# Kernel tuning notes

Measured on AMD Instinct MI355X. Metric: run time of the kernel, lower is better.

Reference implementation:

```python
import jax, jax.numpy as jnp
import numpy as np

N = 100000      # nodes
E = 1600000     # directed edges (before self loops)
F_IN = 128      # n_features
H = 100         # hidden width of every GCNConv / fc1
N_HIDDEN = 8    # conv2..conv9


def setup_inputs() -> dict:
    key = jax.random.key(0)
    ks = jax.random.split(key, 12)
    s = 0.05
    x = jax.random.normal(ks[0], (N, F_IN), jnp.float32)
    edge_index = jax.random.randint(ks[1], (2, E), 0, N, dtype=jnp.int64)
    labels = (jax.random.uniform(ks[2], (N, 1)) < 0.1).astype(jnp.float32)
    W1 = jax.random.normal(ks[3], (F_IN, H), jnp.float32) * s
    b1 = jnp.zeros((H,), jnp.float32)
    Wh = jax.random.normal(ks[4], (N_HIDDEN, H, H), jnp.float32) * s
    bh = jnp.zeros((N_HIDDEN, H), jnp.float32)
    fc1_W = jax.random.normal(ks[5], (H, H), jnp.float32) * s
    fc1_b = jnp.zeros((H,), jnp.float32)
    fc2_W = jax.random.normal(ks[6], (H, 1), jnp.float32) * s
    fc2_b = jnp.zeros((1,), jnp.float32)
    return {"x": x, "edge_index": edge_index, "labels": labels,
            "W1": W1, "b1": b1, "Wh": Wh, "bh": bh,
            "fc1_W": fc1_W, "fc1_b": fc1_b, "fc2_W": fc2_W, "fc2_b": fc2_b}


def _gcn_conv(h, W, b, src, dst, norm):
    # linear transform, then degree-normalized scatter aggregation (PyG GCNConv)
    h = h @ W                                   # [N, H]
    msg = h[src] * norm[:, None]                # [E2, H] gather + scale
    agg = jax.ops.segment_sum(msg, dst, num_segments=N)  # scatter-add to [N, H]
    return agg + b


def reference(x, edge_index, labels, W1, b1, Wh, bh, fc1_W, fc1_b, fc2_W, fc2_b):
    # GCN normalization with self loops: norm_e = deg^-1/2[src] * deg^-1/2[dst]
    loops = jnp.arange(N, dtype=edge_index.dtype)
    src = jnp.concatenate([edge_index[0], loops])
    dst = jnp.concatenate([edge_index[1], loops])
    deg = jax.ops.segment_sum(jnp.ones_like(dst, jnp.float32), dst, num_segments=N)
    dinv = jax.lax.rsqrt(deg)                   # deg >= 1 due to self loops
    norm = dinv[src] * dinv[dst]

    # NOTE: source uses x.relu() (out-of-place, discarded) -> no nonlinearity;
    # dropout is identity in eval mode. Faithful reproduction below.
    h = _gcn_conv(x, W1, b1, src, dst, norm)
    for i in range(N_HIDDEN):
        h = _gcn_conv(h, Wh[i], bh[i], src, dst, norm)

    h = h @ fc1_W + fc1_b
    logits = h @ fc2_W + fc2_b
    p = jax.nn.sigmoid(logits)                  # [N, 1]

    # generate_weights: upweight positives by neg/pos ratio
    pos = labels.sum()
    w = ((jnp.float32(N) - pos) / pos) * labels + 1.0

    pc = jnp.clip(p, 1e-7, 1.0 - 1e-7)
    bce = -(labels * jnp.log(pc) + (1.0 - labels) * jnp.log(1.0 - pc))
    loss = jnp.mean(w * bce)
    return loss, p
```

## Files before the change

### kernel.cpp

```cpp
#include <hip/hip_runtime.h>
#include <hip/hip_fp16.h>
#include <math.h>

#define HW 100
#define FIN 128
#define NBLK 256
#define TPB 1024
#define CHUNK 392
#define PBLK 500
#define SLICE 3200
#define SL4 800
#define ELDS 7424
#define M17 0x1FFFFu
#define NPADH 100352
#define HSPLIT 50048
#define HV40 6256
#define HV41 6244

typedef int iv4 __attribute__((ext_vector_type(4)));

__device__ __forceinline__ float ld_dev(const float* p) {
    return __hip_atomic_load(p, __ATOMIC_RELAXED, __HIP_MEMORY_SCOPE_AGENT);
}
__device__ __forceinline__ unsigned ld_devu(const unsigned* p) {
    return __hip_atomic_load(p, __ATOMIC_RELAXED, __HIP_MEMORY_SCOPE_AGENT);
}
__device__ __forceinline__ void st_devu(unsigned* p, unsigned v) {
    __hip_atomic_store(p, v, __ATOMIC_RELAXED, __HIP_MEMORY_SCOPE_AGENT);
}
__device__ __forceinline__ void st_devh(__half* p, __half v) {
    __hip_atomic_store(reinterpret_cast<unsigned short*>(p),
                       *reinterpret_cast<unsigned short*>(&v),
                       __ATOMIC_RELAXED, __HIP_MEMORY_SCOPE_AGENT);
}

__global__ __launch_bounds__(256) void k_prep(const int* __restrict__ src,
                                              const int* __restrict__ dst,
                                              unsigned* __restrict__ buckets,
                                              int* __restrict__ cntG, int* __restrict__ ofsG,
                                              float* __restrict__ accums,
                                              unsigned* __restrict__ posDone,
                                              unsigned* __restrict__ fin,
                                              unsigned* __restrict__ flags,
                                              const float* __restrict__ W1, const float* __restrict__ b1,
                                              const float* __restrict__ Wh, const float* __restrict__ bh,
                                              const float* __restrict__ fc1W, const float* __restrict__ fc1b,
                                              const float* __restrict__ fc2W, const float* __restrict__ fc2b,
                                              float* __restrict__ wstar, float* __restrict__ gammas) {
    int tid = threadIdx.x;
    if (blockIdx.x == 0) {
        __shared__ float v[HW], vn[HW];
        for (int i = tid; i < NBLK * 16; i += 256) flags[i] = 0u;
        if (tid < HW) v[tid] = fc2W[tid];
        __syncthreads();
        if (tid < HW) { float a = 0.f; for (int c = 0; c < HW; ++c) a += fc1W[tid * HW + c] * v[c]; vn[tid] = a; }
        __syncthreads();
        if (tid < HW) v[tid] = vn[tid];
        __syncthreads();
        if (tid == 0) {
            float a = 0.f; for (int c = 0; c < HW; ++c) a += bh[7 * HW + c] * v[c];
            float b = 0.f; for (int c = 0; c < HW; ++c) b += fc1b[c] * fc2W[c];
            gammas[9] = a + b + fc2b[0];
        }
        __syncthreads();
        for (int i = 7; i >= 0; --i) {
            const float* M = Wh + (size_t)i * HW * HW;
            if (tid < HW) { float a = 0.f; for (int c = 0; c < HW; ++c) a += M[tid * HW + c] * v[c]; vn[tid] = a; }
            __syncthreads();
            if (tid < HW) v[tid] = vn[tid];
            __syncthreads();
            if (tid == 0) {
                const float* bb = (i >= 1) ? (bh + (size_t)(i - 1) * HW) : b1;
                float a = 0.f; for (int c = 0; c < HW; ++c) a += bb[c] * v[c];
                gammas[i + 1] = a;
            }
            __syncthreads();
        }
        if (tid < FIN) { float a = 0.f; for (int c = 0; c < HW; ++c) a += W1[tid * HW + c] * v[c]; wstar[tid] = a; }
        if (tid == 0) { accums[0] = 0.f; accums[1] = 0.f; *posDone = 0u; *fin = 0u; }
        return;
    }
    __shared__ int cur[NBLK], wr[NBLK];
    int p = blockIdx.x - 1;
    if (tid < NBLK) cur[tid] = 0;
    __syncthreads();
    const iv4* d4 = reinterpret_cast<const iv4*>(dst) + (size_t)p * SL4;
    const iv4* s4 = reinterpret_cast<const iv4*>(src) + (size_t)p * SL4;
    for (int i = tid; i < SL4; i += 256) {
        iv4 d = d4[i];
        #pragma unroll
        for (int q = 0; q < 4; ++q) {
            unsigned dd = (unsigned)d[q];
            unsigned c = (unsigned)(((unsigned long long)dd * 171634ull) >> 26);
            atomicAdd(&cur[c], 1);
        }
    }
    __syncthreads();
    {
        __shared__ int sc[NBLK];
        if (tid < NBLK) sc[tid] = cur[tid];
        __syncthreads();
        for (int off = 1; off < NBLK; off <<= 1) {
            int v = (tid < NBLK && tid >= off) ? sc[tid - off] : 0;
            __syncthreads();
            if (tid < NBLK) sc[tid] += v;
            __syncthreads();
        }
        if (tid < NBLK) {
            int o = sc[tid] - cur[tid];
            wr[tid] = o;
            cntG[(size_t)p * NBLK + tid] = cur[tid];
            ofsG[(size_t)p * NBLK + tid] = o;
        }
    }
    __syncthreads();
    unsigned* out = buckets + (size_t)p * SLICE;
    for (int i = tid; i < SL4; i += 256) {
        iv4 d = d4[i];
        iv4 s = s4[i];
        #pragma unroll
        for (int q = 0; q < 4; ++q) {
            unsigned dd = (unsigned)d[q];
            unsigned ss = (unsigned)s[q];
            unsigned c = (unsigned)(((unsigned long long)dd * 171634ull) >> 26);
            unsigned ldst = dd - c * 391u;
            int pos = atomicAdd(&wr[c], 1);
            out[pos] = ss | (ldst << 17);
        }
    }
}

__global__ __launch_bounds__(TPB) void k_main(const float* __restrict__ x,
        const float* __restrict__ labels,
        const float* __restrict__ wstar, const float* __restrict__ gammas,
        const int* __restrict__ cntG, const int* __restrict__ ofsG,
        const unsigned* __restrict__ bucketsG,
        __half* __restrict__ ubase,
        float* __restrict__ accums, unsigned* __restrict__ flags,
        unsigned* __restrict__ posDone, unsigned* __restrict__ fin,
        float* __restrict__ outF, int N) {
    __shared__ alignas(16) float ws[FIN];
    __shared__ float gam[16];
    __shared__ int   cntL[512], incl[512], ofsL[512];
    __shared__ int   degLi[CHUNK];
    __shared__ float dinvL[CHUNK], uownL[CHUNK], yownL[CHUNK], accL[CHUNK];
    __shared__ float red[TPB];
    __shared__ alignas(16) unsigned myE[ELDS];
    __shared__ alignas(16) __half uL[HSPLIT];
    __shared__ int h0c, c0, c1;

    int tid = threadIdx.x;
    int b = blockIdx.x;
    int chunk = (N + NBLK - 1) / NBLK;
    int nlo = b * chunk; if (nlo > N) nlo = N;
    int nhi = nlo + chunk; if (nhi > N) nhi = N;
    int nn = nhi - nlo;

    if (tid < FIN) ws[tid] = wstar[tid];
    if (tid < 16) gam[tid] = gammas[tid];
    for (int r = tid; r < CHUNK; r += TPB) degLi[r] = 0;
    if (tid < 512) {
        int v = (tid < PBLK) ? cntG[(size_t)tid * NBLK + b] : 0;
        cntL[tid] = v; incl[tid] = v;
        ofsL[tid] = (tid < PBLK) ? ofsG[(size_t)tid * NBLK + b] : 0;
    }
    if (tid == 0) { h0c = 0; }
    __syncthreads();
    for (int off = 1; off < 512; off <<= 1) {
        int v = (tid < 512 && tid >= off) ? incl[tid - off] : 0;
        __syncthreads();
        if (tid < 512) incl[tid] += v;
        __syncthreads();
    }
    int ecnt = incl[511];
    if (ecnt > ELDS) ecnt = ELDS;

    for (int p = tid; p < PBLK; p += TPB) {
        int c = cntL[p];
        int g = p * SLICE + ofsL[p];
        int lb = incl[p] - c;
        for (int j = 0; j < c; ++j) {
            unsigned e = bucketsG[g + j];
            if (lb + j < ELDS) { myE[lb + j] = e; atomicAdd(&degLi[e >> 17], 1); }
        }
    }
    __syncthreads();
    {
        unsigned* scr = reinterpret_cast<unsigned*>(uL);
        for (int e = tid; e < ecnt; e += TPB) {
            unsigned v = myE[e];
            scr[e] = v;
            if ((v & M17) < HSPLIT) atomicAdd(&h0c, 1);
        }
        __syncthreads();
        if (tid == 0) { c0 = 0; c1 = h0c; }
        __syncthreads();
        for (int e = tid; e < ecnt; e += TPB) {
            unsigned v = scr[e];
            int pos = ((v & M17) < HSPLIT) ? atomicAdd(&c0, 1) : atomicAdd(&c1, 1);
            myE[pos] = v;
        }
    }
    for (int r = tid; r < nn; r += TPB) dinvL[r] = rsqrtf((float)degLi[r] + 1.0f);
    __syncthreads();
    int seg0 = h0c;

    {
        int wid = tid >> 6, half = (tid >> 5) & 1, l32 = tid & 31;
        int pcnt = (nn + 1) >> 1;
        const float4* x4 = reinterpret_cast<const float4*>(x);
        for (int pb = wid; pb < pcnt; pb += 16) {
            int ln = pb * 2 + half;
            float dsum = 0.f;
            if (ln < nn) {
                float4 xv = x4[(size_t)(nlo + ln) * (FIN / 4) + l32];
                float4 wv = *reinterpret_cast<const float4*>(&ws[l32 * 4]);
                dsum = xv.x * wv.x + xv.y * wv.y + xv.z * wv.z + xv.w * wv.w;
            }
            #pragma unroll
            for (int off = 16; off; off >>= 1) dsum += __shfl_down(dsum, off, 32);
            if (l32 == 0 && ln < nn) {
                float u0 = dsum * dinvL[ln];
                uownL[ln] = u0;
                st_devh(&ubase[nlo + ln], __float2half(u0));
            }
        }
    }
    asm volatile("s_waitcnt vmcnt(0)" ::: "memory");
    {
        float s = 0.f;
        for (int ln = tid; ln < nn; ln += TPB) s += labels[nlo + ln];
        red[tid] = s; __syncthreads();
        for (int off = TPB / 2; off; off >>= 1) {
            if (tid < off) red[tid] += red[tid + off];
            __syncthreads();
        }
        if (tid == 0) {
            atomicAdd(&accums[0], red[0]);
            asm volatile("s_waitcnt vmcnt(0)" ::: "memory");
            __hip_atomic_fetch_add(posDone, 1u, __ATOMIC_RELAXED, __HIP_MEMORY_SCOPE_AGENT);
            st_devu(&flags[b * 16], 1u);
        }
    }

    for (int k = 1; k <= 9; ++k) {
        const __half* ubr = ubase + (size_t)(k - 1) * NPADH;
        __half* ubw = ubase + (size_t)k * NPADH;
        float gk = gam[k];
        for (int ln = tid; ln < nn; ln += TPB) accL[ln] = uownL[ln];
        if (tid < 128)
            while (ld_devu(&flags[tid * 16]) < (unsigned)k) __builtin_amdgcn_s_sleep(16);
        __syncthreads();
        {
            const uint4* sv = reinterpret_cast<const uint4*>(ubr);
            uint4* dv = reinterpret_cast<uint4*>(uL);
            for (int i = tid; i < HV40; i += TPB) dv[i] = sv[i];
        }
        __syncthreads();
        for (int e = tid; e < seg0; e += TPB) {
            unsigned p = myE[e];
            atomicAdd(&accL[p >> 17], __half2float(uL[p & M17]));
        }
        if (tid < 128)
            while (ld_devu(&flags[(128 + tid) * 16]) < (unsigned)k) __builtin_amdgcn_s_sleep(16);
        __syncthreads();
        {
            const uint4* sv = reinterpret_cast<const uint4*>(ubr + HSPLIT);
            uint4* dv = reinterpret_cast<uint4*>(uL);
            for (int i = tid; i < HV41; i += TPB) dv[i] = sv[i];
        }
        __syncthreads();
        for (int e = seg0 + tid; e < ecnt; e += TPB) {
            unsigned p = myE[e];
            atomicAdd(&accL[p >> 17], __half2float(uL[(p & M17) - HSPLIT]));
        }
        __syncthreads();
        for (int ln = tid; ln < nn; ln += TPB) {
            float di = dinvL[ln];
            float y = di * accL[ln] + gk;
            float nu = di * y;
            uownL[ln] = nu;
            if (k < 9) st_devh(&ubw[nlo + ln], __float2half(nu));
            else yownL[ln] = y;
        }
        if (k < 9) {
            asm volatile("s_waitcnt vmcnt(0)" ::: "memory");
            __syncthreads();
            if (tid == 0) st_devu(&flags[b * 16], (unsigned)(k + 1));
        }
    }
    __syncthreads();

    if (tid == 0)
        while (ld_devu(posDone) < NBLK) __builtin_amdgcn_s_sleep(16);
    __syncthreads();
    {
        float pos = ld_dev(&accums[0]);
        float wpos = ((float)N - pos) / pos;
        float acc = 0.f;
        for (int ln = tid; ln < nn; ln += TPB) {
            float y = yownL[ln];
            float pp = 1.f / (1.f + expf(-y));
            outF[1 + nlo + ln] = pp;
            float pc = fminf(fmaxf(pp, 1e-7f), 1.f - 1e-7f);
            float l = labels[nlo + ln];
            float w = wpos * l + 1.f;
            acc += w * (-(l * logf(pc) + (1.f - l) * logf(1.f - pc)));
        }
        red[tid] = acc; __syncthreads();
        for (int off = TPB / 2; off; off >>= 1) {
            if (tid < off) red[tid] += red[tid + off];
            __syncthreads();
        }
        if (tid == 0) {
            atomicAdd(&accums[1], red[0]);
            asm volatile("s_waitcnt vmcnt(0)" ::: "memory");
            unsigned old = __hip_atomic_fetch_add(fin, 1u, __ATOMIC_RELAXED, __HIP_MEMORY_SCOPE_AGENT);
            if (old == NBLK - 1u)
                outF[0] = ld_dev(&accums[1]) / (float)N;
        }
    }
}

extern "C" void kernel_launch(void* const* d_in, const int* in_sizes, int n_in,
                              void* d_out, int out_size, void* d_ws, size_t ws_size,
                              hipStream_t stream) {
    const float* x      = (const float*)d_in[0];
    const int*   edge   = (const int*)d_in[1];
    const float* labels = (const float*)d_in[2];
    const float* W1     = (const float*)d_in[3];
    const float* b1     = (const float*)d_in[4];
    const float* Wh     = (const float*)d_in[5];
    const float* bh     = (const float*)d_in[6];
    const float* fc1W   = (const float*)d_in[7];
    const float* fc1b   = (const float*)d_in[8];
    const float* fc2W   = (const float*)d_in[9];
    const float* fc2b   = (const float*)d_in[10];

    const int N = in_sizes[0] / FIN;
    const int E = in_sizes[1] / 2;
    const int* srcIdx = edge;
    const int* dstIdx = edge + E;

    size_t o = 0;
    auto carve = [&](size_t bytes) {
        void* p = (char*)d_ws + o;
        o += (bytes + 511) & ~(size_t)511;
        return p;
    };
    float*    accums  = (float*)   carve(4 * 4);
    unsigned* posDone = (unsigned*)carve(4);
    unsigned* fin     = (unsigned*)carve(4);
    unsigned* flags   = (unsigned*)carve((size_t)NBLK * 16 * 4);
    float*    wstar   = (float*)   carve(FIN * 4);
    float*    gammas  = (float*)   carve(16 * 4);
    __half*   ubase   = (__half*)  carve((size_t)NPADH * 10 * 2);
    int*      cnt     = (int*)     carve((size_t)PBLK * NBLK * 4);
    int*      ofs     = (int*)     carve((size_t)PBLK * NBLK * 4);
    unsigned* buckets = (unsigned*)carve((size_t)PBLK * SLICE * 4);
    (void)ws_size; (void)n_in; (void)out_size;

    k_prep<<<PBLK + 1, 256, 0, stream>>>(srcIdx, dstIdx, buckets, cnt, ofs,
                                         accums, posDone, fin, flags,
                                         W1, b1, Wh, bh, fc1W, fc1b, fc2W, fc2b,
                                         wstar, gammas);

    float* outF = (float*)d_out;
    int Nv = N;
    void* args[] = {(void*)&x, (void*)&labels, (void*)&wstar, (void*)&gammas,
                    (void*)&cnt, (void*)&ofs, (void*)&buckets, (void*)&ubase,
                    (void*)&accums, (void*)&flags, (void*)&posDone, (void*)&fin,
                    (void*)&outF, (void*)&Nv};
    hipError_t err = hipLaunchCooperativeKernel((const void*)k_main, dim3(NBLK), dim3(TPB),
                                                args, 0, stream);
    (void)err;
}
```

Measured before the change: 218.1 us.

## Replace LDS staging with direct gathers and hierarchical per-layer barrier

Drops the shared-memory copy of each half of the fp16 feature vector and instead gathers neighbour values straight from global memory, unrolled by four. The per-layer wait where 128 threads per block polled every peer flag is replaced by a two-level barrier: blocks 0 and 1 each watch one half of the flags and publish generation counters that the other blocks poll. Edge bucketing is partitioned directly into the two source halves during the load, which removes the extra LDS reorder pass, and the prep partition count is doubled while the slice size is halved. Spin sleep intervals are shortened. The costs are random global-memory reads in place of LDS reads, an extra hop of latency through the two aggregator blocks, and more polling traffic.

```diff
diff --git a/kernel.cpp b/kernel.cpp
--- a/kernel.cpp
+++ b/kernel.cpp
@@ -7,15 +7,13 @@
 #define NBLK 256
 #define TPB 1024
 #define CHUNK 392
-#define PBLK 500
-#define SLICE 3200
-#define SL4 800
+#define PBLK 1000
+#define SLICE 1600
+#define SL4 400
 #define ELDS 7424
 #define M17 0x1FFFFu
 #define NPADH 100352
 #define HSPLIT 50048
-#define HV40 6256
-#define HV41 6244
 
 typedef int iv4 __attribute__((ext_vector_type(4)));
 
@@ -42,6 +40,7 @@
                                               unsigned* __restrict__ posDone,
                                               unsigned* __restrict__ fin,
                                               unsigned* __restrict__ flags,
+                                              unsigned* __restrict__ gens,
                                               const float* __restrict__ W1, const float* __restrict__ b1,
                                               const float* __restrict__ Wh, const float* __restrict__ bh,
                                               const float* __restrict__ fc1W, const float* __restrict__ fc1b,
@@ -51,6 +50,7 @@
     if (blockIdx.x == 0) {
         __shared__ float v[HW], vn[HW];
         for (int i = tid; i < NBLK * 16; i += 256) flags[i] = 0u;
+        if (tid < 256) gens[tid] = 0u;
         if (tid < HW) v[tid] = fc2W[tid];
         __syncthreads();
         if (tid < HW) { float a = 0.f; for (int c = 0; c < HW; ++c) a += fc1W[tid * HW + c] * v[c]; vn[tid] = a; }
@@ -137,18 +137,20 @@
         const unsigned* __restrict__ bucketsG,
         __half* __restrict__ ubase,
         float* __restrict__ accums, unsigned* __restrict__ flags,
+        unsigned* __restrict__ gens,
         unsigned* __restrict__ posDone, unsigned* __restrict__ fin,
         float* __restrict__ outF, int N) {
     __shared__ alignas(16) float ws[FIN];
     __shared__ float gam[16];
-    __shared__ int   cntL[512], incl[512], ofsL[512];
+    __shared__ int   cntL[1024], incl[1024], ofsL[1024];
     __shared__ int   degLi[CHUNK];
     __shared__ float dinvL[CHUNK], uownL[CHUNK], yownL[CHUNK], accL[CHUNK];
     __shared__ float red[TPB];
     __shared__ alignas(16) unsigned myE[ELDS];
-    __shared__ alignas(16) __half uL[HSPLIT];
-    __shared__ int h0c, c0, c1;
-
+    __shared__ int cA, cB;
+
+    unsigned* genA = gens;
+    unsigned* genB = gens + 128;
     int tid = threadIdx.x;
     int b = blockIdx.x;
     int chunk = (N + NBLK - 1) / NBLK;
@@ -159,51 +161,43 @@
     if (tid < FIN) ws[tid] = wstar[tid];
     if (tid < 16) gam[tid] = gammas[tid];
     for (int r = tid; r < CHUNK; r += TPB) degLi[r] = 0;
-    if (tid < 512) {
+    {
         int v = (tid < PBLK) ? cntG[(size_t)tid * NBLK + b] : 0;
         cntL[tid] = v; incl[tid] = v;
         ofsL[tid] = (tid < PBLK) ? ofsG[(size_t)tid * NBLK + b] : 0;
     }
-    if (tid == 0) { h0c = 0; }
-    __syncthreads();
-    for (int off = 1; off < 512; off <<= 1) {
-        int v = (tid < 512 && tid >= off) ? incl[tid - off] : 0;
-        __syncthreads();
-        if (tid < 512) incl[tid] += v;
-        __syncthreads();
-    }
-    int ecnt = incl[511];
+    __syncthreads();
+    for (int off = 1; off < 1024; off <<= 1) {
+        int v = (tid >= off) ? incl[tid - off] : 0;
+        __syncthreads();
+        incl[tid] += v;
+        __syncthreads();
+    }
+    int ecnt = incl[1023];
     if (ecnt > ELDS) ecnt = ELDS;
+    if (tid == 0) { cA = 0; cB = ecnt; }
+    __syncthreads();
 
     for (int p = tid; p < PBLK; p += TPB) {
         int c = cntL[p];
+        if (c == 0) continue;
         int g = p * SLICE + ofsL[p];
-        int lb = incl[p] - c;
+        int nA = 0;
+        for (int j = 0; j < c; ++j) nA += ((bucketsG[g + j] & M17) < HSPLIT) ? 1 : 0;
+        int nB = c - nA;
+        int baseA = atomicAdd(&cA, nA);
+        int baseB = atomicAdd(&cB, -nB) - nB;
+        int ia = 0, ib = 0;
         for (int j = 0; j < c; ++j) {
             unsigned e = bucketsG[g + j];
-            if (lb + j < ELDS) { myE[lb + j] = e; atomicAdd(&degLi[e >> 17], 1); }
-        }
-    }
-    __syncthreads();
-    {
-        unsigned* scr = reinterpret_cast<unsigned*>(uL);
-        for (int e = tid; e < ecnt; e += TPB) {
-            unsigned v = myE[e];
-            scr[e] = v;
-            if ((v & M17) < HSPLIT) atomicAdd(&h0c, 1);
-        }
-        __syncthreads();
-        if (tid == 0) { c0 = 0; c1 = h0c; }
-        __syncthreads();
-        for (int e = tid; e < ecnt; e += TPB) {
-            unsigned v = scr[e];
-            int pos = ((v & M17) < HSPLIT) ? atomicAdd(&c0, 1) : atomicAdd(&c1, 1);
-            myE[pos] = v;
-        }
-    }
+            int pos = ((e & M17) < HSPLIT) ? (baseA + ia++) : (baseB + ib++);
+            if (pos >= 0 && pos < ELDS) { myE[pos] = e; atomicAdd(&degLi[e >> 17], 1); }
+        }
+    }
+    __syncthreads();
+    int seg0 = cA;
     for (int r = tid; r < nn; r += TPB) dinvL[r] = rsqrtf((float)degLi[r] + 1.0f);
     __syncthreads();
-    int seg0 = h0c;
 
     {
         int wid = tid >> 6, half = (tid >> 5) & 1, l32 = tid & 31;
@@ -248,31 +242,70 @@
         __half* ubw = ubase + (size_t)k * NPADH;
         float gk = gam[k];
         for (int ln = tid; ln < nn; ln += TPB) accL[ln] = uownL[ln];
-        if (tid < 128)
-            while (ld_devu(&flags[tid * 16]) < (unsigned)k) __builtin_amdgcn_s_sleep(16);
+        unsigned kk = (unsigned)k;
+        if (b == 0) {
+            for (int j = tid; j < 128; j += TPB)
+                while (ld_devu(&flags[j * 16]) < kk) __builtin_amdgcn_s_sleep(2);
+            __syncthreads();
+            if (tid < 8) st_devu(&genA[tid * 16], kk);
+        } else if (b == 1) {
+            for (int j = tid; j < 128; j += TPB)
+                while (ld_devu(&flags[(128 + j) * 16]) < kk) __builtin_amdgcn_s_sleep(2);
+            __syncthreads();
+            if (tid < 8) st_devu(&genB[tid * 16], kk);
+            if (tid == 0)
+                while (ld_devu(&genA[(b & 7) * 16]) < kk) __builtin_amdgcn_s_sleep(2);
+        } else {
+            if (tid == 0)
+                while (ld_devu(&genA[(b & 7) * 16]) < kk) __builtin_amdgcn_s_sleep(2);
+        }
         __syncthreads();
         {
-            const uint4* sv = reinterpret_cast<const uint4*>(ubr);
-            uint4* dv = reinterpret_cast<uint4*>(uL);
-            for (int i = tid; i < HV40; i += TPB) dv[i] = sv[i];
-        }
-        __syncthreads();
-        for (int e = tid; e < seg0; e += TPB) {
-            unsigned p = myE[e];
-            atomicAdd(&accL[p >> 17], __half2float(uL[p & M17]));
-        }
-        if (tid < 128)
-            while (ld_devu(&flags[(128 + tid) * 16]) < (unsigned)k) __builtin_amdgcn_s_sleep(16);
+            int len = seg0;
+            int l4 = len & ~3;
+            for (int i = tid * 4; i < l4; i += TPB * 4) {
+                unsigned p0 = myE[i], p1 = myE[i + 1], p2 = myE[i + 2], p3 = myE[i + 3];
+                float f0 = __half2float(ubr[p0 & M17]);
+                float f1 = __half2float(ubr[p1 & M17]);
+                float f2 = __half2float(ubr[p2 & M17]);
+                float f3 = __half2float(ubr[p3 & M17]);
+                atomicAdd(&accL[p0 >> 17], f0);
+                atomicAdd(&accL[p1 >> 17], f1);
+                atomicAdd(&accL[p2 >> 17], f2);
+                atomicAdd(&accL[p3 >> 17], f3);
+            }
+            for (int i = l4 + tid; i < len; i += TPB) {
+                unsigned p = myE[i];
+                atomicAdd(&accL[p >> 17], __half2float(ubr[p & M17]));
+            }
+        }
+        if (b == 0) {
+            if (tid == 0)
+                while (ld_devu(&genB[0]) < kk) __builtin_amdgcn_s_sleep(2);
+        } else if (b != 1) {
+            if (tid == 0)
+                while (ld_devu(&genB[(b & 7) * 16]) < kk) __builtin_amdgcn_s_sleep(2);
+        }
         __syncthreads();
         {
-            const uint4* sv = reinterpret_cast<const uint4*>(ubr + HSPLIT);
-            uint4* dv = reinterpret_cast<uint4*>(uL);
-            for (int i = tid; i < HV41; i += TPB) dv[i] = sv[i];
-        }
-        __syncthreads();
-        for (int e = seg0 + tid; e < ecnt; e += TPB) {
-            unsigned p = myE[e];
-            atomicAdd(&accL[p >> 17], __half2float(uL[(p & M17) - HSPLIT]));
+            int len = ecnt - seg0;
+            int l4 = len & ~3;
+            for (int i = tid * 4; i < l4; i += TPB * 4) {
+                unsigned p0 = myE[seg0 + i], p1 = myE[seg0 + i + 1];
+                unsigned p2 = myE[seg0 + i + 2], p3 = myE[seg0 + i + 3];
+                float f0 = __half2float(ubr[p0 & M17]);
+                float f1 = __half2float(ubr[p1 & M17]);
+                float f2 = __half2float(ubr[p2 & M17]);
+                float f3 = __half2float(ubr[p3 & M17]);
+                atomicAdd(&accL[p0 >> 17], f0);
+                atomicAdd(&accL[p1 >> 17], f1);
+                atomicAdd(&accL[p2 >> 17], f2);
+                atomicAdd(&accL[p3 >> 17], f3);
+            }
+            for (int i = l4 + tid; i < len; i += TPB) {
+                unsigned p = myE[seg0 + i];
+                atomicAdd(&accL[p >> 17], __half2float(ubr[p & M17]));
+            }
         }
         __syncthreads();
         for (int ln = tid; ln < nn; ln += TPB) {
@@ -286,13 +319,13 @@
         if (k < 9) {
             asm volatile("s_waitcnt vmcnt(0)" ::: "memory");
             __syncthreads();
-            if (tid == 0) st_devu(&flags[b * 16], (unsigned)(k + 1));
+            if (tid == 0) st_devu(&flags[b * 16], kk + 1u);
         }
     }
     __syncthreads();
 
     if (tid == 0)
-        while (ld_devu(posDone) < NBLK) __builtin_amdgcn_s_sleep(16);
+        while (ld_devu(posDone) < NBLK) __builtin_amdgcn_s_sleep(2);
     __syncthreads();
     {
         float pos = ld_dev(&accums[0]);
@@ -352,16 +385,17 @@
     unsigned* posDone = (unsigned*)carve(4);
     unsigned* fin     = (unsigned*)carve(4);
     unsigned* flags   = (unsigned*)carve((size_t)NBLK * 16 * 4);
+    unsigned* gens    = (unsigned*)carve(256 * 4);
     float*    wstar   = (float*)   carve(FIN * 4);
     float*    gammas  = (float*)   carve(16 * 4);
     __half*   ubase   = (__half*)  carve((size_t)NPADH * 10 * 2);
     int*      cnt     = (int*)     carve((size_t)PBLK * NBLK * 4);
     int*      ofs     = (int*)     carve((size_t)PBLK * NBLK * 4);
     unsigned* buckets = (unsigned*)carve((size_t)PBLK * SLICE * 4);
-    (void)ws_size; (void)n_in; (void)out_size;
+    (void)ws_size; (void)n_in; (void)out_size; (void)E;
 
     k_prep<<<PBLK + 1, 256, 0, stream>>>(srcIdx, dstIdx, buckets, cnt, ofs,
-                                         accums, posDone, fin, flags,
+                                         accums, posDone, fin, flags, gens,
                                          W1, b1, Wh, bh, fc1W, fc1b, fc2W, fc2b,
                                          wstar, gammas);
 
@@ -369,8 +403,8 @@
     int Nv = N;
     void* args[] = {(void*)&x, (void*)&labels, (void*)&wstar, (void*)&gammas,
                     (void*)&cnt, (void*)&ofs, (void*)&buckets, (void*)&ubase,
-                    (void*)&accums, (void*)&flags, (void*)&posDone, (void*)&fin,
-                    (void*)&outF, (void*)&Nv};
+                    (void*)&accums, (void*)&flags, (void*)&gens,
+                    (void*)&posDone, (void*)&fin, (void*)&outF, (void*)&Nv};
     hipError_t err = hipLaunchCooperativeKernel((const void*)k_main, dim3(NBLK), dim3(TPB),
                                                 args, 0, stream);
     (void)err;
```

Result: faster. 200.2 us (-8.2%).
